# Performance work log

Measured on AMD Instinct MI355X. Metric: run time of the kernel, lower is better.

## Reference

```python
import jax, jax.numpy as jnp
import numpy as np

N = 30000      # nodes
E = 480000     # edges
H = 128        # hidden_nf
NQ = 7         # qubits
D = 2 ** NQ    # 128, quantum state dim == embedding_size
NL = 2         # block n_layers (QGCL layers)
QL = 2         # quantum circuit layers inside each QGCL
NORM = 100.0   # normalization_factor ('sum' aggregation)
NORM_CONST = 1.0


def _cnot_perm_indices(n):
    # Composed permutation for CNOT(0,1)...CNOT(n-2,n-1), CNOT(n-1,0).
    # PennyLane convention: wire 0 is the most significant bit.
    idx = np.arange(2 ** n)
    pairs = [(i, i + 1) for i in range(n - 1)] + [(n - 1, 0)]
    g = None
    for c, t in pairs:
        cb = (idx >> (n - 1 - c)) & 1
        f = idx ^ (cb << (n - 1 - t))  # flip target bit if control set (involution)
        g = f if g is None else g[f]
    return g

_CNOT_G = jnp.asarray(_cnot_perm_indices(NQ))


def _quantum_states(q_in, coeffs, A_re, A_im):
    """Vectorized VQC over all nodes. q_in [N,D] real -> [N,D] complex state."""
    norm = jnp.sqrt(jnp.sum(q_in ** 2, axis=1, keepdims=True) + 1e-12)
    s = (q_in / norm).astype(jnp.complex64)  # normalized initial state per node
    I = jnp.eye(D, dtype=jnp.complex64)
    for j in range(QL):
        # Cayley transform -> unitary
        A = (A_re[j] + 1j * A_im[j]).astype(jnp.complex64)
        A = A + A.conj().T
        q = (A - 1j * I) @ jnp.linalg.inv(A + 1j * I)
        # single-qubit layer: RY(b) @ RX(a) on every qubit -> kron power
        a, b = coeffs[j, 0].astype(jnp.complex64), coeffs[j, 1].astype(jnp.complex64)
        ca, sa = jnp.cos(a / 2), jnp.sin(a / 2)
        cb, sb = jnp.cos(b / 2), jnp.sin(b / 2)
        RX = jnp.stack([jnp.stack([ca, -1j * sa]), jnp.stack([-1j * sa, ca])])
        RY = jnp.stack([jnp.stack([cb, -sb]), jnp.stack([sb, cb])])
        G = RY @ RX
        Gk = G
        for _ in range(NQ - 1):
            Gk = jnp.kron(Gk, G)
        s = s @ q.T            # QubitUnitary
        s = s @ Gk.T           # RX/RY on all qubits
        s = s[:, _CNOT_G]      # CNOT ring (pure permutation)
    return s


def setup_inputs() -> dict:
    key = jax.random.key(0)
    ks = jax.random.split(key, 20)
    return {
        "h": jax.random.normal(ks[0], (N, H), jnp.float32),
        "x": jax.random.normal(ks[1], (N, 3), jnp.float32),
        "edge_index": jax.random.randint(ks[2], (2, E), 0, N, jnp.int32),
        "edge_attr": jax.random.normal(ks[3], (E, 1), jnp.float32),
        "e_w1": jax.random.normal(ks[4], (NL, 2 * H + 2, H), jnp.float32) * 0.05,
        "e_b1": jnp.zeros((NL, H), jnp.float32),
        "e_w2": jax.random.normal(ks[5], (NL, H, H), jnp.float32) * 0.05,
        "e_b2": jnp.zeros((NL, H), jnp.float32),
        "enc_w": jax.random.normal(ks[6], (NL, 2 * H, D), jnp.float32) * 0.05,
        "enc_b": jnp.zeros((NL, D), jnp.float32),
        "coeffs": jax.random.normal(ks[7], (NL, QL, 2), jnp.float32) * 0.1,
        "A_re": jax.random.normal(ks[8], (NL, QL, D, D), jnp.float32) * 0.01,
        "A_im": jax.random.normal(ks[9], (NL, QL, D, D), jnp.float32) * 0.01,
        "dec_w": jax.random.normal(ks[10], (NL, D, H), jnp.float32) * 0.05,
        "dec_b": jnp.zeros((NL, H), jnp.float32),
        "c_w1": jax.random.normal(ks[11], (2 * H + 2, H), jnp.float32) * 0.05,
        "c_b1": jnp.zeros((H,), jnp.float32),
        "c_w2": jax.random.normal(ks[12], (H, H), jnp.float32) * 0.05,
        "c_b2": jnp.zeros((H,), jnp.float32),
        "c_w3": jax.random.normal(ks[13], (H, 1), jnp.float32) * 0.001,  # xavier gain=0.001
    }


def reference(h, x, edge_index, edge_attr, e_w1, e_b1, e_w2, e_b2, enc_w, enc_b,
              coeffs, A_re, A_im, dec_w, dec_b, c_w1, c_b1, c_w2, c_b2, c_w3):
    row, col = edge_index[0], edge_index[1]
    # coord2diff
    diff = x[row] - x[col]
    radial = jnp.sum(diff ** 2, axis=1, keepdims=True)     # [E,1] (used as 'distances')
    coord_diff = diff / (jnp.sqrt(radial + 1e-8) + NORM_CONST)
    eattr = jnp.concatenate([radial, edge_attr], axis=1)   # [E,2]

    for l in range(NL):  # QGCL layers
        m = jnp.concatenate([h[row], h[col], eattr], axis=1)       # [E, 2H+2]
        m = jax.nn.silu(m @ e_w1[l] + e_b1[l])
        m = jax.nn.silu(m @ e_w2[l] + e_b2[l])                     # edge messages mij
        agg = jax.ops.segment_sum(m, row, num_segments=N) / NORM   # scatter-add
        q_in = jnp.concatenate([h, agg], axis=1) @ enc_w[l] + enc_b[l]
        # quantum part is detached in the original (torch .detach + re-tensor)
        qs = jax.lax.stop_gradient(
            _quantum_states(q_in, coeffs[l], A_re[l], A_im[l]))
        h = h + qs.real.astype(h.dtype) @ dec_w[l] + dec_b[l]

    # EquivariantUpdate (tanh=False)
    t = jnp.concatenate([h[row], h[col], eattr], axis=1)
    t = jax.nn.silu(t @ c_w1 + c_b1)
    t = jax.nn.silu(t @ c_w2 + c_b2)
    t = t @ c_w3                                                   # [E,1]
    trans = coord_diff * t
    x = x + jax.ops.segment_sum(trans, row, num_segments=N) / NORM
    return h, x
```

## Files before the change

### kernel.cpp

```cpp
#include <hip/hip_runtime.h>
#include <math.h>

#define N_NODES 30000
#define N_EDGES 480000
#define HDIM 128
#define EPB 64
#define NAS 264
#define MS 136
#define M2S 132

typedef __attribute__((ext_vector_type(8))) short short8b;
typedef __attribute__((ext_vector_type(4))) float f32x4;

__device__ __forceinline__ float silu_f(float v) {
  return v / (1.0f + __expf(-v));
}

__device__ __forceinline__ unsigned short f2bf(float f) {
  unsigned int u = __float_as_uint(f);
  unsigned int r = u + 0x7fffu + ((u >> 16) & 1u);
  return (unsigned short)(r >> 16);
}

__device__ __forceinline__ unsigned int cvt_pk_bf16(float lo, float hi) {
  unsigned int r;
  asm("v_cvt_pk_bf16_f32 %0, %1, %2" : "=v"(r) : "v"(lo), "v"(hi));
  return r;
}

__global__ void init_out_bf_kernel(const float* __restrict__ h,
                                   const float* __restrict__ x,
                                   const int* __restrict__ ei,
                                   float* __restrict__ out,
                                   ushort* __restrict__ hbf,
                                   int* __restrict__ cursor) {
  int idx = blockIdx.x * 256 + threadIdx.x;
  float4 v = ((const float4*)h)[idx];
  ((float4*)out)[idx] = v;
  ushort4 o;
  o.x = f2bf(v.x); o.y = f2bf(v.y); o.z = f2bf(v.z); o.w = f2bf(v.w);
  ((ushort4*)hbf)[idx] = o;
  if (idx < N_NODES * 3 / 4) {
    ((float4*)(out + N_NODES * HDIM))[idx] = ((const float4*)x)[idx];
  }
  if (idx < N_EDGES) atomicAdd(&cursor[ei[idx]], 1);
}

__global__ __launch_bounds__(1024) void scan_kernel(int* __restrict__ cursor,
                                                    int* __restrict__ cstart) {
  __shared__ int sums[1024];
  const int tid = threadIdx.x;
  const int base = tid * 30;
  int local[30];
  int s = 0;
#pragma unroll
  for (int j = 0; j < 30; ++j) {
    int idx = base + j;
    int d = (idx < N_NODES) ? cursor[idx] : 0;
    local[j] = s;
    s += d;
  }
  sums[tid] = s;
  __syncthreads();
  for (int off = 1; off < 1024; off <<= 1) {
    int add = (tid >= off) ? sums[tid - off] : 0;
    __syncthreads();
    sums[tid] += add;
    __syncthreads();
  }
  int excl = (tid == 0) ? 0 : sums[tid - 1];
#pragma unroll
  for (int j = 0; j < 30; ++j) {
    int idx = base + j;
    if (idx < N_NODES) {
      int v = excl + local[j];
      cursor[idx] = v;
      cstart[idx] = v;
    }
  }
}

__global__ void prep_kernel(
    const int* __restrict__ ei, int* __restrict__ cursor, int* __restrict__ elist,
    const float* __restrict__ e_w1, const float* __restrict__ e_w2,
    const float* __restrict__ enc_w, const float* __restrict__ c_w1,
    const float* __restrict__ c_w2,
    ushort* __restrict__ w1cs, ushort* __restrict__ w2cs,
    ushort* __restrict__ enccs, ushort* __restrict__ cw1cs,
    ushort* __restrict__ cw2cs,
    const float* __restrict__ A_re, const float* __restrict__ A_im,
    float2* __restrict__ X,
    const float* __restrict__ coeffs, float2* __restrict__ gkm) {
  const int b = blockIdx.x, tid = threadIdx.x;
  if (b < 1875) {
    int e = b * 256 + tid;
    int r = ei[e];
    int pos = atomicAdd(&cursor[r], 1);
    elist[pos] = e;
  } else if (b < 2755) {
    int idx = (b - 1875) * 256 + tid;
    int ci = idx >> 12, rem = idx & 4095, kk = rem & 31;
    const float* W; ushort* dst; int Kreal, ktl;
    if (ci < 18) {
      int l = ci / 9; ktl = ci - l * 9;
      W = e_w1 + (size_t)l * 258 * HDIM; dst = w1cs + (size_t)l * 9 * 4096;
      Kreal = 258;
    } else if (ci < 26) {
      int c2 = ci - 18; int l = c2 >> 2; ktl = c2 & 3;
      W = e_w2 + (size_t)l * HDIM * HDIM; dst = w2cs + (size_t)l * 4 * 4096;
      Kreal = 128;
    } else if (ci < 42) {
      int c2 = ci - 26; int l = c2 >> 3; ktl = c2 & 7;
      W = enc_w + (size_t)l * 256 * HDIM; dst = enccs + (size_t)l * 8 * 4096;
      Kreal = 256;
    } else if (ci < 51) {
      ktl = ci - 42; W = c_w1; dst = cw1cs; Kreal = 258;
    } else {
      ktl = ci - 51; W = c_w2; dst = cw2cs; Kreal = 128;
    }
    int n = rem >> 5;
    int k = ktl * 32 + kk;
    float v = (k < Kreal) ? W[(size_t)k * HDIM + n] : 0.0f;
    dst[ktl * 4096 + rem] = f2bf(v);
  } else if (b < 3011) {
    int bb = b - 2755;
    int lj = bb >> 6;
    int idx = (bb & 63) * 256 + tid;
    int r = idx >> 7, c = idx & 127;
    const float* are = A_re + (size_t)lj * 16384;
    const float* aim = A_im + (size_t)lj * 16384;
    float re = are[r * 128 + c] + are[c * 128 + r];
    float im = aim[r * 128 + c] - aim[c * 128 + r];
    if (r == c) im -= 1.0f;
    X[(size_t)lj * 16384 + idx] = make_float2(re, im);
  } else {
    int bb = b - 3011;
    int lj = bb >> 6;
    float a = coeffs[lj * 2 + 0], bcf = coeffs[lj * 2 + 1];
    float ca = cosf(0.5f * a), sa = sinf(0.5f * a);
    float cb = cosf(0.5f * bcf), sb = sinf(0.5f * bcf);
    float2 G[2][2];
    G[0][0] = make_float2(cb * ca, sb * sa);
    G[0][1] = make_float2(-sb * ca, -cb * sa);
    G[1][0] = make_float2(sb * ca, -cb * sa);
    G[1][1] = make_float2(cb * ca, -sb * sa);
    int idx = (bb & 63) * 256 + tid;
    int r = idx >> 7, c = idx & 127;
    float2 acc = make_float2(1.f, 0.f);
#pragma unroll
    for (int bit = 6; bit >= 0; --bit) {
      float2 g = G[(r >> bit) & 1][(c >> bit) & 1];
      acc = make_float2(acc.x * g.x - acc.y * g.y, acc.x * g.y + acc.y * g.x);
    }
    gkm[(size_t)lj * 16384 + idx] = acc;
  }
}

__global__ void ns_bx_kernel(const float* __restrict__ Are,
                             const float* __restrict__ Aim,
                             const float2* __restrict__ X,
                             float2* __restrict__ T) {
  int lj = blockIdx.y;
  int idx = blockIdx.x * 256 + threadIdx.x;
  int r = idx >> 7, c = idx & 127;
  const float* are = Are + (size_t)lj * 16384;
  const float* aim = Aim + (size_t)lj * 16384;
  const float2* x = X + (size_t)lj * 16384;
  float2 acc = make_float2(0.f, 0.f);
  for (int k = 0; k < 128; ++k) {
    float re = are[r * 128 + k] + are[k * 128 + r];
    float im = aim[r * 128 + k] - aim[k * 128 + r];
    if (k == r) im += 1.0f;
    float2 b = x[k * 128 + c];
    acc.x += re * b.x - im * b.y;
    acc.y += re * b.y + im * b.x;
  }
  T[(size_t)lj * 16384 + idx] = acc;
}

__global__ void ns_upd_kernel(const float2* __restrict__ X,
                              const float2* __restrict__ T,
                              float2* __restrict__ Xn) {
  int lj = blockIdx.y;
  int idx = blockIdx.x * 256 + threadIdx.x;
  int r = idx >> 7, c = idx & 127;
  const float2* x = X + (size_t)lj * 16384;
  const float2* t = T + (size_t)lj * 16384;
  float2 acc = make_float2(0.f, 0.f);
  for (int k = 0; k < 128; ++k) {
    float2 a = x[r * 128 + k];
    float2 b = t[k * 128 + c];
    acc.x += a.x * b.x - a.y * b.y;
    acc.y += a.x * b.y + a.y * b.x;
  }
  float2 xc = x[r * 128 + c];
  Xn[(size_t)lj * 16384 + idx] = make_float2(2.f * xc.x - acc.x, 2.f * xc.y - acc.y);
}

__global__ void qmat_kernel(const float* __restrict__ Are,
                            const float* __restrict__ Aim,
                            const float2* __restrict__ binvg,
                            float2* __restrict__ qm) {
  int lj = blockIdx.y;
  int idx = blockIdx.x * 256 + threadIdx.x;
  int r = idx >> 7, c = idx & 127;
  const float* are = Are + (size_t)lj * 16384;
  const float* aim = Aim + (size_t)lj * 16384;
// ... 20 lines not shown
  {
    int v = c;
    const int cs[7] = {6, 5, 4, 3, 2, 1, 0};
    const int ts[7] = {0, 6, 5, 4, 3, 2, 1};
#pragma unroll
    for (int p = 0; p < 7; ++p) {
      int cb = (v >> (6 - cs[p])) & 1;
      v = v ^ (cb << (6 - ts[p]));
    }
    gc = v;
  }
  const float2* q = qm + (size_t)lj * 16384;
  const float2* gk = gkm + (size_t)lj * 16384;
  float2 acc = make_float2(0.f, 0.f);
  for (int k = 0; k < 128; ++k) {
    float2 qa = q[k * 128 + i];
    float2 gb = gk[gc * 128 + k];
    acc.x += qa.x * gb.x - qa.y * gb.y;
    acc.y += qa.x * gb.y + qa.y * gb.x;
  }
  njm[(size_t)lj * 16384 + idx] = acc;
}

__global__ void compose_kernel(const float2* __restrict__ njm,
                               float2* __restrict__ um) {
  int l = blockIdx.y;
  int idx = blockIdx.x * 256 + threadIdx.x;
  int i = idx >> 7, c = idx & 127;
  const float2* n0 = njm + (size_t)(l * 2 + 0) * 16384;
  const float2* n1 = njm + (size_t)(l * 2 + 1) * 16384;
  float2 acc = make_float2(0.f, 0.f);
  for (int k = 0; k < 128; ++k) {
    float2 a = n0[i * 128 + k];
    float2 b = n1[k * 128 + c];
    acc.x += a.x * b.x - a.y * b.y;
    acc.y += a.x * b.y + a.y * b.x;
  }
  um[(size_t)l * 16384 + idx] = acc;
}

__global__ void wqd_kernel(const float2* __restrict__ um,
                           const float* __restrict__ decw,
                           ushort* __restrict__ wqdcs) {
  int l = blockIdx.y;
  int idx = blockIdx.x * 256 + threadIdx.x;
  int i = idx >> 7, c = idx & 127;
  const float2* u = um + (size_t)l * 16384;
  const float* dw = decw + (size_t)l * 16384;
  float acc = 0.f;
  for (int k = 0; k < 128; ++k) acc += u[i * 128 + k].x * dw[k * 128 + c];
  wqdcs[(size_t)l * 4 * 4096 + (i >> 5) * 4096 + c * 32 + (i & 31)] = f2bf(acc);
}

__global__ __launch_bounds__(256, 1) void pgemm_kernel(
    const ushort* __restrict__ hbf, const ushort* __restrict__ wcs,
    const float* __restrict__ b1, ushort* __restrict__ P) {
  __shared__ ushort Ht[EPB * MS];
  const int tid = threadIdx.x;
  const int n0 = blockIdx.x * EPB;
  const int lane = tid & 63, wave = tid >> 6;
  const int lrow = lane & 15, lq = lane >> 4;

  {
    const int e = tid >> 2, jj = tid & 3;
    int node = n0 + e;
    if (node >= N_NODES) node = N_NODES - 1;
    const uint4* src = (const uint4*)(hbf + (size_t)node * HDIM + jj * 32);
    uint4* dst = (uint4*)(Ht + e * MS + jj * 32);
    dst[0] = src[0]; dst[1] = src[1]; dst[2] = src[2]; dst[3] = src[3];
  }
  short8b wf[4][4];
  const int cs = (wave >> 1) * 4;
  const int nb = (wave & 1) * 64;
#pragma unroll
  for (int kt = 0; kt < 4; ++kt)
#pragma unroll
    for (int nt = 0; nt < 4; ++nt)
      wf[kt][nt] = *(const short8b*)(wcs + (cs + kt) * 4096 + (nb + nt * 16 + lrow) * 32 + lq * 8);
  __syncthreads();

  f32x4 acc[4][4];
#pragma unroll
  for (int mt = 0; mt < 4; ++mt)
#pragma unroll
    for (int nt = 0; nt < 4; ++nt) acc[mt][nt] = (f32x4){0.f, 0.f, 0.f, 0.f};
#pragma unroll
  for (int kt = 0; kt < 4; ++kt) {
    short8b af[4];
#pragma unroll
    for (int mt = 0; mt < 4; ++mt)
      af[mt] = *(const short8b*)(Ht + (mt * 16 + lrow) * MS + kt * 32 + lq * 8);
#pragma unroll
    for (int mt = 0; mt < 4; ++mt)
#pragma unroll
      for (int nt = 0; nt < 4; ++nt)
        acc[mt][nt] = __builtin_amdgcn_mfma_f32_16x16x32_bf16(af[mt], wf[kt][nt], acc[mt][nt], 0, 0, 0);
  }
  const int cbase = wave * 64;
#pragma unroll
  for (int nt = 0; nt < 4; ++nt) {
    const int ccol = cbase + nt * 16 + lrow;
    const float bb = (ccol < 128) ? b1[ccol] : 0.f;
#pragma unroll
    for (int mt = 0; mt < 4; ++mt)
#pragma unroll
      for (int r = 0; r < 4; ++r) {
        const int node = n0 + mt * 16 + lq * 4 + r;
        if (node < N_NODES) P[(size_t)node * 256 + ccol] = f2bf(acc[mt][nt][r] + bb);
      }
  }
}

__global__ __launch_bounds__(256, 4) void edge_mfma_kernel(
    const ushort* __restrict__ P, const int* __restrict__ ei,
    const float* __restrict__ x, const float* __restrict__ ea,
    const int* __restrict__ elist, const int* __restrict__ cstart,
    const float* __restrict__ wm,
    const ushort* __restrict__ w2cs, const float* __restrict__ b2,
    float* __restrict__ agg, float* __restrict__ headp) {
  __shared__ float m2s[EPB * M2S];
  __shared__ int rows[EPB];
  ushort* m1 = (ushort*)m2s;

  const int tid = threadIdx.x;
  const int lane = tid & 63, wave = tid >> 6;
  const int lrow = lane & 15, lq = lane >> 4;
  const int wbase = wave * 32;
  const int woff0 = (wbase + lrow) * 32 + lq * 8;
  const int woff1 = (wbase + 16 + lrow) * 32 + lq * 8;
  const float b2v[2] = {b2[wbase + lrow], b2[wbase + 16 + lrow]};

  const int i0 = blockIdx.x * EPB;
  {
    const int e = tid >> 2, j = tid & 3;
    const int edge = elist[i0 + e];
    const int r = ei[edge], c = ei[N_EDGES + edge];
    if (j == 0) rows[e] = r;
    const uint4* pr = (const uint4*)(P + (size_t)r * 256 + j * 32);
    const uint4* pc = (const uint4*)(P + (size_t)c * 256 + 128 + j * 32);
    uint4 PR[4] = {pr[0], pr[1], pr[2], pr[3]};
    uint4 PC[4] = {pc[0], pc[1], pc[2], pc[3]};
    float dx = x[r * 3 + 0] - x[c * 3 + 0];
    float dy = x[r * 3 + 1] - x[c * 3 + 1];
    float dz = x[r * 3 + 2] - x[c * 3 + 2];
    float radial = dx * dx + dy * dy + dz * dz;
    float eav = ea[edge];
#pragma unroll
    for (int q = 0; q < 4; ++q) {
      const int kb = j * 32 + q * 8;
      const uint ua[4] = {PR[q].x, PR[q].y, PR[q].z, PR[q].w};
      const uint ub[4] = {PC[q].x, PC[q].y, PC[q].z, PC[q].w};
      uint ow[4];
#pragma unroll
      for (int w = 0; w < 4; ++w) {
        const int k = kb + w * 2;
        float v0 = __uint_as_float(ua[w] << 16) + __uint_as_float(ub[w] << 16)
                 + radial * wm[k] + eav * wm[128 + k];
        float v1 = __uint_as_float(ua[w] & 0xffff0000u) + __uint_as_float(ub[w] & 0xffff0000u)
                 + radial * wm[k + 1] + eav * wm[129 + k];
        ow[w] = cvt_pk_bf16(silu_f(v0), silu_f(v1));
      }
      uint4 o; o.x = ow[0]; o.y = ow[1]; o.z = ow[2]; o.w = ow[3];
      *(uint4*)(m1 + e * MS + kb) = o;
    }
  }
  __syncthreads();

  f32x4 acc2[4][2];
#pragma unroll
  for (int mt = 0; mt < 4; ++mt)
#pragma unroll
    for (int nt = 0; nt < 2; ++nt) acc2[mt][nt] = (f32x4){0.f, 0.f, 0.f, 0.f};
  {
    short8b wcur0 = *(const short8b*)(w2cs + woff0);
    short8b wcur1 = *(const short8b*)(w2cs + woff1);
#pragma unroll
    for (int kt = 0; kt < 4; ++kt) {
      short8b wn0, wn1;
      if (kt < 3) {
        wn0 = *(const short8b*)(w2cs + (kt + 1) * 4096 + woff0);
        wn1 = *(const short8b*)(w2cs + (kt + 1) * 4096 + woff1);
      }
      short8b af[4];
#pragma unroll
      for (int mt = 0; mt < 4; ++mt)
        af[mt] = *(const short8b*)(m1 + (mt * 16 + lrow) * MS + kt * 32 + lq * 8);
#pragma unroll
      for (int mt = 0; mt < 4; ++mt) {
        acc2[mt][0] = __builtin_amdgcn_mfma_f32_16x16x32_bf16(af[mt], wcur0, acc2[mt][0], 0, 0, 0);
        acc2[mt][1] = __builtin_amdgcn_mfma_f32_16x16x32_bf16(af[mt], wcur1, acc2[mt][1], 0, 0, 0);
      }
      if (kt < 3) { wcur0 = wn0; wcur1 = wn1; }
    }
  }
  __syncthreads();
#pragma unroll
  for (int mt = 0; mt < 4; ++mt)
#pragma unroll
    for (int nt = 0; nt < 2; ++nt)
#pragma unroll
      for (int r = 0; r < 4; ++r)
        m2s[(mt * 16 + lq * 4 + r) * M2S + wbase + nt * 16 + lrow] =
            silu_f(acc2[mt][nt][r] + b2v[nt]);
  __syncthreads();

  const int e2 = tid & 63, cg = tid >> 6, cb = cg * 32;
  if (((e2 & 1) == 0) && (rows[e2 + 1] == rows[e2])) {
    float* d = m2s + e2 * M2S + cb;
    const float* s = m2s + (e2 + 1) * M2S + cb;
#pragma unroll
    for (int q = 0; q < 8; ++q)
      *(f32x4*)(d + q * 4) = *(const f32x4*)(d + q * 4) + *(const f32x4*)(s + q * 4);
  }
  __syncthreads();
  if (((e2 & 3) == 0) && (rows[e2 + 2] == rows[e2])) {
    float* d = m2s + e2 * M2S + cb;
    const float* s = m2s + (e2 + 2) * M2S + cb;
#pragma unroll
    for (int q = 0; q < 8; ++q)
      *(f32x4*)(d + q * 4) = *(const f32x4*)(d + q * 4) + *(const f32x4*)(s + q * 4);
  }
  __syncthreads();
  const int r_e = rows[e2];
  const bool leader = (e2 == 0) || (rows[e2 - 1] != r_e);
  if (leader) {
    f32x4 sum[8];
#pragma unroll
    for (int q = 0; q < 8; ++q) sum[q] = *(const f32x4*)(m2s + e2 * M2S + cb + q * 4);
    int f = e2 + ((e2 & 1) ? 1 : ((e2 & 2) ? 2 : 4));
    while (f < EPB && rows[f] == r_e) {
#pragma unroll
      for (int q = 0; q < 8; ++q) sum[q] += *(const f32x4*)(m2s + f * M2S + cb + q * 4);
      f += (f & 1) ? 1 : ((f & 2) ? 2 : 4);
    }
    float* dst = (e2 == 0 && cstart[r_e] < i0)
                     ? headp + (size_t)blockIdx.x * HDIM + cb
                     : agg + (size_t)r_e * HDIM + cb;
#pragma unroll
    for (int q = 0; q < 8; ++q) *(f32x4*)(dst + q * 4) = sum[q];
  }
}

__global__ __launch_bounds__(256, 2) void node_mfma_kernel(
    float* __restrict__ out_h, const float* __restrict__ agg,
    const int* __restrict__ cstart, const int* __restrict__ cend,
    const float* __restrict__ headp,
    const ushort* __restrict__ enccs, const float* __restrict__ encb,
    const ushort* __restrict__ wqdcs, const float* __restrict__ decb,
    ushort* __restrict__ hbf) {
  __shared__ ushort A[EPB * NAS];
  __shared__ ushort m1[EPB * MS];
  __shared__ float nbuf[4 * EPB];
  const int tid = threadIdx.x;
  const int n0 = blockIdx.x * EPB;

  const int lane = tid & 63, wave = tid >> 6;
  const int lrow = lane & 15, lq = lane >> 4;
  const int wbase = wave * 32;

  short8b wef[8][2], wqf[4][2];
#pragma unroll
  for (int kt = 0; kt < 8; ++kt)
#pragma unroll
    for (int nt = 0; nt < 2; ++nt)
      wef[kt][nt] = *(const short8b*)(enccs + kt * 4096 + (wbase + nt * 16 + lrow) * 32 + lq * 8);
#pragma unroll
  for (int kt = 0; kt < 4; ++kt)
#pragma unroll
    for (int nt = 0; nt < 2; ++nt)
      wqf[kt][nt] = *(const short8b*)(wqdcs + kt * 4096 + (wbase + nt * 16 + lrow) * 32 + lq * 8);
  const float ebv[2] = {encb[wbase + lrow], encb[wbase + 16 + lrow]};
  const float dbv[2] = {decb[wbase + lrow], decb[wbase + 16 + lrow]};

  {
    const int e = tid >> 2, j = tid & 3;
    int node = n0 + e;
    if (node >= N_NODES) node = N_NODES - 1;
    if (j < 2) {
      const float4* s4 = (const float4*)(out_h + (size_t)node * HDIM + j * 64);
      ushort* dst = A + e * NAS + j * 64;
#pragma unroll
      for (int i = 0; i < 16; ++i) {
        float4 v = s4[i];
        ushort4 o;
        o.x = f2bf(v.x); o.y = f2bf(v.y); o.z = f2bf(v.z); o.w = f2bf(v.w);
        ((ushort4*)dst)[i] = o;
      }
    } else {
      const int s = cstart[node], en = cend[node];
      const bool hasAgg = en > s;
      const float4* a4 = (const float4*)(agg + (size_t)node * HDIM + (j - 2) * 64);
      const int bb0 = (s >> 6) + 1;
      const int bb1 = hasAgg ? ((en - 1) >> 6) : 0;
      ushort* dst = A + e * NAS + 128 + (j - 2) * 64;
#pragma unroll
      for (int i = 0; i < 16; ++i) {
        float4 v = hasAgg ? a4[i] : make_float4(0.f, 0.f, 0.f, 0.f);
        for (int bb = bb0; bb <= bb1; ++bb) {
          float4 hv = *(const float4*)(headp + (size_t)bb * HDIM + (j - 2) * 64 + i * 4);
          v.x += hv.x; v.y += hv.y; v.z += hv.z; v.w += hv.w;
        }
        ushort4 o;
// ... 23 lines not shown
        acc[mt][nt] = __builtin_amdgcn_mfma_f32_16x16x32_bf16(af[mt], wef[kt][nt], acc[mt][nt], 0, 0, 0);
  }
#pragma unroll
  for (int mt = 0; mt < 4; ++mt) {
    float ssp[4] = {0.f, 0.f, 0.f, 0.f};
#pragma unroll
    for (int nt = 0; nt < 2; ++nt)
#pragma unroll
      for (int r = 0; r < 4; ++r) {
        acc[mt][nt][r] += ebv[nt];
        ssp[r] += acc[mt][nt][r] * acc[mt][nt][r];
      }
#pragma unroll
    for (int m = 1; m < 16; m <<= 1)
#pragma unroll
      for (int r = 0; r < 4; ++r) ssp[r] += __shfl_xor(ssp[r], m, 64);
    if (lrow == 0) {
#pragma unroll
      for (int r = 0; r < 4; ++r)
        nbuf[wave * EPB + mt * 16 + lq * 4 + r] = ssp[r];
    }
  }
  __syncthreads();
#pragma unroll
  for (int mt = 0; mt < 4; ++mt)
#pragma unroll
    for (int r = 0; r < 4; ++r) {
      const int row = mt * 16 + lq * 4 + r;
      float sum = nbuf[row] + nbuf[EPB + row] + nbuf[2 * EPB + row] + nbuf[3 * EPB + row];
      float inv = 1.0f / sqrtf(sum + 1e-12f);
#pragma unroll
      for (int nt = 0; nt < 2; ++nt)
        m1[row * MS + wbase + nt * 16 + lrow] = f2bf(acc[mt][nt][r] * inv);
    }
  __syncthreads();

  f32x4 acc2[4][2];
#pragma unroll
  for (int mt = 0; mt < 4; ++mt)
#pragma unroll
    for (int nt = 0; nt < 2; ++nt) acc2[mt][nt] = (f32x4){0.f, 0.f, 0.f, 0.f};
#pragma unroll
  for (int kt = 0; kt < 4; ++kt) {
    short8b af[4];
#pragma unroll
    for (int mt = 0; mt < 4; ++mt)
      af[mt] = *(const short8b*)(m1 + (mt * 16 + lrow) * MS + kt * 32 + lq * 8);
#pragma unroll
    for (int mt = 0; mt < 4; ++mt)
#pragma unroll
      for (int nt = 0; nt < 2; ++nt)
        acc2[mt][nt] = __builtin_amdgcn_mfma_f32_16x16x32_bf16(af[mt], wqf[kt][nt], acc2[mt][nt], 0, 0, 0);
  }
#pragma unroll
  for (int mt = 0; mt < 4; ++mt)
#pragma unroll
    for (int nt = 0; nt < 2; ++nt) {
      const int n = wbase + nt * 16 + lrow;
#pragma unroll
      for (int r = 0; r < 4; ++r) {
        const int node = n0 + mt * 16 + lq * 4 + r;
        if (node < N_NODES) {
          size_t off = (size_t)node * HDIM + n;
          float hn = out_h[off] + acc2[mt][nt][r] + dbv[nt];
          out_h[off] = hn;
          hbf[off] = f2bf(hn);
        }
      }
    }
}

__global__ __launch_bounds__(256, 4) void coord_mfma_kernel(
    const ushort* __restrict__ P, const int* __restrict__ ei,
    const float* __restrict__ x, const float* __restrict__ ea,
    const int* __restrict__ elist,
    const float* __restrict__ wm,
    const ushort* __restrict__ w2cs, const float* __restrict__ b2,
    const float* __restrict__ w3, float* __restrict__ xout) {
  __shared__ ushort m1[EPB * MS];
  __shared__ int rows[EPB];
  __shared__ float pbuf[4 * EPB];
  __shared__ float tv[EPB];
  __shared__ float dxs[EPB], dys[EPB], dzs[EPB], ses[EPB];

  const int tid = threadIdx.x;
  const int lane = tid & 63, wave = tid >> 6;
  const int lrow = lane & 15, lq = lane >> 4;
  const int wbase = wave * 32;
  const int woff0 = (wbase + lrow) * 32 + lq * 8;
  const int woff1 = (wbase + 16 + lrow) * 32 + lq * 8;

  const float b2v[2] = {b2[wbase + lrow], b2[wbase + 16 + lrow]};
  const float w3v[2] = {w3[wbase + lrow], w3[wbase + 16 + lrow]};

  const int i0 = blockIdx.x * EPB;
  {
    const int e = tid >> 2, j = tid & 3;
    const int edge = elist[i0 + e];
    const int r = ei[edge], c = ei[N_EDGES + edge];
    if (j == 0) rows[e] = r;
    const uint4* pr = (const uint4*)(P + (size_t)r * 256 + j * 32);
    const uint4* pc = (const uint4*)(P + (size_t)c * 256 + 128 + j * 32);
    uint4 PR[4] = {pr[0], pr[1], pr[2], pr[3]};
    uint4 PC[4] = {pc[0], pc[1], pc[2], pc[3]};
    float dx = x[r * 3 + 0] - x[c * 3 + 0];
    float dy = x[r * 3 + 1] - x[c * 3 + 1];
    float dz = x[r * 3 + 2] - x[c * 3 + 2];
    float radial = dx * dx + dy * dy + dz * dz;
    float eav = ea[edge];
    if (j == 3) {
      dxs[e] = dx; dys[e] = dy; dzs[e] = dz;
      ses[e] = 1.0f / (sqrtf(radial + 1e-8f) + 1.0f);
    }
#pragma unroll
    for (int q = 0; q < 4; ++q) {
      const int kb = j * 32 + q * 8;
      const uint ua[4] = {PR[q].x, PR[q].y, PR[q].z, PR[q].w};
      const uint ub[4] = {PC[q].x, PC[q].y, PC[q].z, PC[q].w};
      uint ow[4];
#pragma unroll
      for (int w = 0; w < 4; ++w) {
        const int k = kb + w * 2;
        float v0 = __uint_as_float(ua[w] << 16) + __uint_as_float(ub[w] << 16)
                 + radial * wm[k] + eav * wm[128 + k];
        float v1 = __uint_as_float(ua[w] & 0xffff0000u) + __uint_as_float(ub[w] & 0xffff0000u)
                 + radial * wm[k + 1] + eav * wm[129 + k];
        ow[w] = cvt_pk_bf16(silu_f(v0), silu_f(v1));
      }
      uint4 o; o.x = ow[0]; o.y = ow[1]; o.z = ow[2]; o.w = ow[3];
      *(uint4*)(m1 + e * MS + kb) = o;
    }
  }
  __syncthreads();

  f32x4 acc2[4][2];
#pragma unroll
  for (int mt = 0; mt < 4; ++mt)
#pragma unroll
    for (int nt = 0; nt < 2; ++nt) acc2[mt][nt] = (f32x4){0.f, 0.f, 0.f, 0.f};
  {
    short8b wcur0 = *(const short8b*)(w2cs + woff0);
    short8b wcur1 = *(const short8b*)(w2cs + woff1);
#pragma unroll
    for (int kt = 0; kt < 4; ++kt) {
      short8b wn0, wn1;
      if (kt < 3) {
        wn0 = *(const short8b*)(w2cs + (kt + 1) * 4096 + woff0);
        wn1 = *(const short8b*)(w2cs + (kt + 1) * 4096 + woff1);
      }
      short8b af[4];
#pragma unroll
      for (int mt = 0; mt < 4; ++mt)
        af[mt] = *(const short8b*)(m1 + (mt * 16 + lrow) * MS + kt * 32 + lq * 8);
#pragma unroll
      for (int mt = 0; mt < 4; ++mt) {
        acc2[mt][0] = __builtin_amdgcn_mfma_f32_16x16x32_bf16(af[mt], wcur0, acc2[mt][0], 0, 0, 0);
        acc2[mt][1] = __builtin_amdgcn_mfma_f32_16x16x32_bf16(af[mt], wcur1, acc2[mt][1], 0, 0, 0);
      }
      if (kt < 3) { wcur0 = wn0; wcur1 = wn1; }
    }
  }
#pragma unroll
  for (int mt = 0; mt < 4; ++mt) {
// ... 15 lines not shown
  }
  __syncthreads();
  if (tid < EPB) {
    tv[tid] = (pbuf[tid] + pbuf[EPB + tid] + pbuf[2 * EPB + tid] + pbuf[3 * EPB + tid])
              * 0.01f * ses[tid];
  }
  __syncthreads();
  if (tid < EPB) {
    const int e = tid;
    const int r_e = rows[e];
    const bool leader = (e == 0) || (rows[e - 1] != r_e);
    if (leader) {
      float sx = 0.f, sy = 0.f, sz = 0.f;
      int f = e;
      do {
        float t = tv[f];
        sx += dxs[f] * t; sy += dys[f] * t; sz += dzs[f] * t;
        ++f;
      } while (f < EPB && rows[f] == r_e);
      atomicAdd(&xout[r_e * 3 + 0], sx);
      atomicAdd(&xout[r_e * 3 + 1], sy);
      atomicAdd(&xout[r_e * 3 + 2], sz);
    }
  }
}

extern "C" void kernel_launch(void* const* d_in, const int* in_sizes, int n_in,
                              void* d_out, int out_size, void* d_ws, size_t ws_size,
                              hipStream_t stream) {
  const float* h     = (const float*)d_in[0];
  const float* x     = (const float*)d_in[1];
  const int*   ei    = (const int*)d_in[2];
  const float* ea    = (const float*)d_in[3];
  const float* e_w1  = (const float*)d_in[4];
  const float* e_b1  = (const float*)d_in[5];
  const float* e_w2  = (const float*)d_in[6];
  const float* e_b2  = (const float*)d_in[7];
  const float* enc_w = (const float*)d_in[8];
  const float* enc_b = (const float*)d_in[9];
  const float* coeffs= (const float*)d_in[10];
  const float* A_re  = (const float*)d_in[11];
  const float* A_im  = (const float*)d_in[12];
  const float* dec_w = (const float*)d_in[13];
  const float* dec_b = (const float*)d_in[14];
  const float* c_w1  = (const float*)d_in[15];
  const float* c_b1  = (const float*)d_in[16];
  const float* c_w2  = (const float*)d_in[17];
  const float* c_b2  = (const float*)d_in[18];
  const float* c_w3  = (const float*)d_in[19];

  float* out = (float*)d_out;
  float* ws  = (float*)d_ws;

  float*  agg    = ws;
  float2* xa     = (float2*)(ws + 3840000);
  float2* xb     = (float2*)(ws + 3971072);
  float2* xt     = (float2*)(ws + 4102144);
  float2* qm     = (float2*)(ws + 4233216);
  float2* gkm    = (float2*)(ws + 4364288);
  float2* njm    = (float2*)(ws + 4495360);
  float2* um     = (float2*)(ws + 4626432);
  int*    cursor = (int*)(ws + 4724864);
  int*    cstart = (int*)(ws + 4754864);
  int*    elist  = (int*)(ws + 4784864);
  float*  headp  = ws + 5264864;
  ushort* hbf    = (ushort*)(ws + 6224864);
  ushort* w1cs   = (ushort*)(ws + 8144864);
  ushort* w2cs   = (ushort*)(ws + 8181728);
  ushort* cw1cs  = (ushort*)(ws + 8198112);
  ushort* cw2cs  = (ushort*)(ws + 8216544);
  ushort* enccs  = (ushort*)(ws + 8224736);
  ushort* wqdcs  = (ushort*)(ws + 8257504);
  ushort* Pbuf   = (ushort*)(ws + 8273888);

  hipMemsetAsync(cursor, 0, N_NODES * sizeof(int), stream);
  init_out_bf_kernel<<<3750, 256, 0, stream>>>(h, x, ei, out, hbf, cursor);
  scan_kernel<<<1, 1024, 0, stream>>>(cursor, cstart);

  prep_kernel<<<3267, 256, 0, stream>>>(ei, cursor, elist,
                                        e_w1, e_w2, enc_w, c_w1, c_w2,
                                        w1cs, w2cs, enccs, cw1cs, cw2cs,
                                        A_re, A_im, xa, coeffs, gkm);

  float2* cur = xa;
  float2* nxt = xb;
  for (int it = 0; it < 2; ++it) {
    ns_bx_kernel<<<dim3(64, 4), 256, 0, stream>>>(A_re, A_im, cur, xt);
    ns_upd_kernel<<<dim3(64, 4), 256, 0, stream>>>(cur, xt, nxt);
    float2* tmp = cur; cur = nxt; nxt = tmp;
  }
  qmat_kernel<<<dim3(64, 4), 256, 0, stream>>>(A_re, A_im, cur, qm);
  nj_kernel<<<dim3(64, 4), 256, 0, stream>>>(qm, gkm, njm);
  compose_kernel<<<dim3(64, 2), 256, 0, stream>>>(njm, um);
  wqd_kernel<<<dim3(64, 2), 256, 0, stream>>>(um, dec_w, wqdcs);

  const int NB = (N_NODES + EPB - 1) / EPB;

  for (int l = 0; l < 2; ++l) {
    pgemm_kernel<<<NB, 256, 0, stream>>>(hbf, w1cs + (size_t)l * 9 * 4096,
                                         e_b1 + l * HDIM, Pbuf);
    edge_mfma_kernel<<<N_EDGES / EPB, 256, 0, stream>>>(
        Pbuf, ei, x, ea, elist, cstart,
        e_w1 + (size_t)l * 258 * HDIM + 256 * HDIM,
        w2cs + (size_t)l * 4 * 4096, e_b2 + l * HDIM, agg, headp);
    node_mfma_kernel<<<NB, 256, 0, stream>>>(
        out, agg, cstart, cursor, headp,
        enccs + (size_t)l * 8 * 4096, enc_b + l * HDIM,
        wqdcs + (size_t)l * 4 * 4096, dec_b + l * HDIM, hbf);
  }

  pgemm_kernel<<<NB, 256, 0, stream>>>(hbf, cw1cs, c_b1, Pbuf);
  coord_mfma_kernel<<<N_EDGES / EPB, 256, 0, stream>>>(
      Pbuf, ei, x, ea, elist, c_w1 + 256 * HDIM, cw2cs, c_b2, c_w3,
      out + (size_t)N_NODES * HDIM);
}
```

Measured before the change: 697.7 us.

## Fuse node projections into prep/node kernels, pack edge data, MFMA segment reduce

Removes the standalone pgemm kernel. The first projection now runs as extra blocks in prep_kernel, and the later ones run at the tail of node_mfma_kernel, which writes the next P buffer directly. Edge sorting now stores packed row/col indices and precomputed radial/edge_attr pairs in sorted order, so the edge kernels skip the indirection and the x gathers. The edge kernel's shared-memory tree reduction by row is replaced with a bf16 one-hot segment-sum matrix multiply on MFMA. The messages are now summed in bf16 rather than fp32 before aggregation, which adds some precision loss.

```diff
diff --git a/kernel.cpp b/kernel.cpp
--- a/kernel.cpp
+++ b/kernel.cpp
@@ -7,7 +7,7 @@
 #define EPB 64
 #define NAS 264
 #define MS 136
-#define M2S 132
+#define M2TS 72
 
 typedef __attribute__((ext_vector_type(8))) short short8b;
 typedef __attribute__((ext_vector_type(4))) float f32x4;
@@ -32,14 +32,9 @@
                                    const float* __restrict__ x,
                                    const int* __restrict__ ei,
                                    float* __restrict__ out,
-                                   ushort* __restrict__ hbf,
                                    int* __restrict__ cursor) {
   int idx = blockIdx.x * 256 + threadIdx.x;
-  float4 v = ((const float4*)h)[idx];
-  ((float4*)out)[idx] = v;
-  ushort4 o;
-  o.x = f2bf(v.x); o.y = f2bf(v.y); o.z = f2bf(v.z); o.w = f2bf(v.w);
-  ((ushort4*)hbf)[idx] = o;
+  ((float4*)out)[idx] = ((const float4*)h)[idx];
   if (idx < N_NODES * 3 / 4) {
     ((float4*)(out + N_NODES * HDIM))[idx] = ((const float4*)x)[idx];
   }
@@ -81,7 +76,9 @@
 }
 
 __global__ void prep_kernel(
-    const int* __restrict__ ei, int* __restrict__ cursor, int* __restrict__ elist,
+    const int* __restrict__ ei, int* __restrict__ cursor,
+    unsigned int* __restrict__ rcp, float2* __restrict__ era,
+    const float* __restrict__ x, const float* __restrict__ ea,
     const float* __restrict__ e_w1, const float* __restrict__ e_w2,
     const float* __restrict__ enc_w, const float* __restrict__ c_w1,
     const float* __restrict__ c_w2,
@@ -90,13 +87,21 @@
     ushort* __restrict__ cw2cs,
     const float* __restrict__ A_re, const float* __restrict__ A_im,
     float2* __restrict__ X,
-    const float* __restrict__ coeffs, float2* __restrict__ gkm) {
+    const float* __restrict__ coeffs, float2* __restrict__ gkm,
+    const float* __restrict__ outh, const float* __restrict__ b1l0,
+    ushort* __restrict__ P) {
+  __shared__ ushort Ht[EPB * MS];
   const int b = blockIdx.x, tid = threadIdx.x;
   if (b < 1875) {
     int e = b * 256 + tid;
     int r = ei[e];
+    int c = ei[N_EDGES + e];
     int pos = atomicAdd(&cursor[r], 1);
-    elist[pos] = e;
+    rcp[pos] = (unsigned int)r | ((unsigned int)c << 16);
+    float dx = x[r * 3 + 0] - x[c * 3 + 0];
+    float dy = x[r * 3 + 1] - x[c * 3 + 1];
+    float dz = x[r * 3 + 2] - x[c * 3 + 2];
+    era[pos] = make_float2(dx * dx + dy * dy + dz * dz, ea[e]);
   } else if (b < 2755) {
     int idx = (b - 1875) * 256 + tid;
     int ci = idx >> 12, rem = idx & 4095, kk = rem & 31;
@@ -133,7 +138,7 @@
     float im = aim[r * 128 + c] - aim[c * 128 + r];
     if (r == c) im -= 1.0f;
     X[(size_t)lj * 16384 + idx] = make_float2(re, im);
-  } else {
+  } else if (b < 3267) {
     int bb = b - 3011;
     int lj = bb >> 6;
     float a = coeffs[lj * 2 + 0], bcf = coeffs[lj * 2 + 1];
@@ -153,6 +158,64 @@
       acc = make_float2(acc.x * g.x - acc.y * g.y, acc.x * g.y + acc.y * g.x);
     }
     gkm[(size_t)lj * 16384 + idx] = acc;
+  } else {
+    const int n0 = (b - 3267) * EPB;
+    const int lane = tid & 63, wave = tid >> 6;
+    const int lrow = lane & 15, lq = lane >> 4;
+    {
+      const int e = tid >> 2, jj = tid & 3;
+      int node = n0 + e;
+      if (node >= N_NODES) node = N_NODES - 1;
+      const float4* s4 = (const float4*)(outh + (size_t)node * HDIM + jj * 32);
+      ushort* dst = Ht + e * MS + jj * 32;
+#pragma unroll
+      for (int i = 0; i < 8; ++i) {
+        float4 v = s4[i];
+        ushort4 o;
+        o.x = f2bf(v.x); o.y = f2bf(v.y); o.z = f2bf(v.z); o.w = f2bf(v.w);
+        ((ushort4*)dst)[i] = o;
+      }
+    }
+    short8b wf[4][4];
+    const int cs = (wave >> 1) * 4;
+    const int nb = (wave & 1) * 64;
+#pragma unroll
+    for (int kt = 0; kt < 4; ++kt)
+#pragma unroll
+      for (int nt = 0; nt < 4; ++nt)
+        wf[kt][nt] = *(const short8b*)(w1cs + (cs + kt) * 4096 + (nb + nt * 16 + lrow) * 32 + lq * 8);
+    __syncthreads();
+
+    f32x4 acc[4][4];
+#pragma unroll
+    for (int mt = 0; mt < 4; ++mt)
+#pragma unroll
+      for (int nt = 0; nt < 4; ++nt) acc[mt][nt] = (f32x4){0.f, 0.f, 0.f, 0.f};
+#pragma unroll
+    for (int kt = 0; kt < 4; ++kt) {
+      short8b af[4];
+#pragma unroll
+      for (int mt = 0; mt < 4; ++mt)
+        af[mt] = *(const short8b*)(Ht + (mt * 16 + lrow) * MS + kt * 32 + lq * 8);
+#pragma unroll
+      for (int mt = 0; mt < 4; ++mt)
+#pragma unroll
+        for (int nt = 0; nt < 4; ++nt)
+          acc[mt][nt] = __builtin_amdgcn_mfma_f32_16x16x32_bf16(af[mt], wf[kt][nt], acc[mt][nt], 0, 0, 0);
+    }
+    const int cbase = wave * 64;
+#pragma unroll
+    for (int nt = 0; nt < 4; ++nt) {
+      const int ccol = cbase + nt * 16 + lrow;
+      const float bb2 = (ccol < 128) ? b1l0[ccol] : 0.f;
+#pragma unroll
+      for (int mt = 0; mt < 4; ++mt)
+#pragma unroll
+        for (int r = 0; r < 4; ++r) {
+          const int node = n0 + mt * 16 + lq * 4 + r;
+          if (node < N_NODES) P[(size_t)node * 256 + ccol] = f2bf(acc[mt][nt][r] + bb2);
+        }
+    }
   }
 }
 
@@ -279,75 +342,19 @@
   wqdcs[(size_t)l * 4 * 4096 + (i >> 5) * 4096 + c * 32 + (i & 31)] = f2bf(acc);
 }
 
-__global__ __launch_bounds__(256, 1) void pgemm_kernel(
-    const ushort* __restrict__ hbf, const ushort* __restrict__ wcs,
-    const float* __restrict__ b1, ushort* __restrict__ P) {
-  __shared__ ushort Ht[EPB * MS];
-  const int tid = threadIdx.x;
-  const int n0 = blockIdx.x * EPB;
-  const int lane = tid & 63, wave = tid >> 6;
-  const int lrow = lane & 15, lq = lane >> 4;
-
-  {
-    const int e = tid >> 2, jj = tid & 3;
-    int node = n0 + e;
-    if (node >= N_NODES) node = N_NODES - 1;
-    const uint4* src = (const uint4*)(hbf + (size_t)node * HDIM + jj * 32);
-    uint4* dst = (uint4*)(Ht + e * MS + jj * 32);
-    dst[0] = src[0]; dst[1] = src[1]; dst[2] = src[2]; dst[3] = src[3];
-  }
-  short8b wf[4][4];
-  const int cs = (wave >> 1) * 4;
-  const int nb = (wave & 1) * 64;
-#pragma unroll
-  for (int kt = 0; kt < 4; ++kt)
-#pragma unroll
-    for (int nt = 0; nt < 4; ++nt)
-      wf[kt][nt] = *(const short8b*)(wcs + (cs + kt) * 4096 + (nb + nt * 16 + lrow) * 32 + lq * 8);
-  __syncthreads();
-
-  f32x4 acc[4][4];
-#pragma unroll
-  for (int mt = 0; mt < 4; ++mt)
-#pragma unroll
-    for (int nt = 0; nt < 4; ++nt) acc[mt][nt] = (f32x4){0.f, 0.f, 0.f, 0.f};
-#pragma unroll
-  for (int kt = 0; kt < 4; ++kt) {
-    short8b af[4];
-#pragma unroll
-    for (int mt = 0; mt < 4; ++mt)
-      af[mt] = *(const short8b*)(Ht + (mt * 16 + lrow) * MS + kt * 32 + lq * 8);
-#pragma unroll
-    for (int mt = 0; mt < 4; ++mt)
-#pragma unroll
-      for (int nt = 0; nt < 4; ++nt)
-        acc[mt][nt] = __builtin_amdgcn_mfma_f32_16x16x32_bf16(af[mt], wf[kt][nt], acc[mt][nt], 0, 0, 0);
-  }
-  const int cbase = wave * 64;
-#pragma unroll
-  for (int nt = 0; nt < 4; ++nt) {
-    const int ccol = cbase + nt * 16 + lrow;
-    const float bb = (ccol < 128) ? b1[ccol] : 0.f;
-#pragma unroll
-    for (int mt = 0; mt < 4; ++mt)
-#pragma unroll
-      for (int r = 0; r < 4; ++r) {
-        const int node = n0 + mt * 16 + lq * 4 + r;
-        if (node < N_NODES) P[(size_t)node * 256 + ccol] = f2bf(acc[mt][nt][r] + bb);
-      }
-  }
-}
-
 __global__ __launch_bounds__(256, 4) void edge_mfma_kernel(
-    const ushort* __restrict__ P, const int* __restrict__ ei,
-    const float* __restrict__ x, const float* __restrict__ ea,
-    const int* __restrict__ elist, const int* __restrict__ cstart,
+    const ushort* __restrict__ P, const unsigned int* __restrict__ rcp,
+    const float2* __restrict__ era, const int* __restrict__ cstart,
     const float* __restrict__ wm,
     const ushort* __restrict__ w2cs, const float* __restrict__ b2,
     float* __restrict__ agg, float* __restrict__ headp) {
-  __shared__ float m2s[EPB * M2S];
+  __shared__ ushort buf[128 * M2TS];
   __shared__ int rows[EPB];
-  ushort* m1 = (ushort*)m2s;
+  __shared__ __align__(16) ushort segv[EPB];
+  __shared__ int segnode[EPB];
+  __shared__ int scont, snseg;
+  ushort* m1 = buf;
+  ushort* m2t = buf;
 
   const int tid = threadIdx.x;
   const int lane = tid & 63, wave = tid >> 6;
@@ -360,18 +367,15 @@
   const int i0 = blockIdx.x * EPB;
   {
     const int e = tid >> 2, j = tid & 3;
-    const int edge = elist[i0 + e];
-    const int r = ei[edge], c = ei[N_EDGES + edge];
+    const unsigned int rcv = rcp[i0 + e];
+    const int r = (int)(rcv & 0xFFFFu), c = (int)(rcv >> 16);
     if (j == 0) rows[e] = r;
+    const float2 re2 = era[i0 + e];
+    const float radial = re2.x, eav = re2.y;
     const uint4* pr = (const uint4*)(P + (size_t)r * 256 + j * 32);
     const uint4* pc = (const uint4*)(P + (size_t)c * 256 + 128 + j * 32);
     uint4 PR[4] = {pr[0], pr[1], pr[2], pr[3]};
     uint4 PC[4] = {pc[0], pc[1], pc[2], pc[3]};
-    float dx = x[r * 3 + 0] - x[c * 3 + 0];
-    float dy = x[r * 3 + 1] - x[c * 3 + 1];
-    float dz = x[r * 3 + 2] - x[c * 3 + 2];
-    float radial = dx * dx + dy * dy + dz * dz;
-    float eav = ea[edge];
 #pragma unroll
     for (int q = 0; q < 4; ++q) {
       const int kb = j * 32 + q * 8;
@@ -421,50 +425,86 @@
     }
   }
   __syncthreads();
+
 #pragma unroll
   for (int mt = 0; mt < 4; ++mt)
 #pragma unroll
-    for (int nt = 0; nt < 2; ++nt)
-#pragma unroll
-      for (int r = 0; r < 4; ++r)
-        m2s[(mt * 16 + lq * 4 + r) * M2S + wbase + nt * 16 + lrow] =
-            silu_f(acc2[mt][nt][r] + b2v[nt]);
-  __syncthreads();
-
-  const int e2 = tid & 63, cg = tid >> 6, cb = cg * 32;
-  if (((e2 & 1) == 0) && (rows[e2 + 1] == rows[e2])) {
-    float* d = m2s + e2 * M2S + cb;
-    const float* s = m2s + (e2 + 1) * M2S + cb;
-#pragma unroll
-    for (int q = 0; q < 8; ++q)
-      *(f32x4*)(d + q * 4) = *(const f32x4*)(d + q * 4) + *(const f32x4*)(s + q * 4);
-  }
-  __syncthreads();
-  if (((e2 & 3) == 0) && (rows[e2 + 2] == rows[e2])) {
-    float* d = m2s + e2 * M2S + cb;
-    const float* s = m2s + (e2 + 2) * M2S + cb;
-#pragma unroll
-    for (int q = 0; q < 8; ++q)
-      *(f32x4*)(d + q * 4) = *(const f32x4*)(d + q * 4) + *(const f32x4*)(s + q * 4);
-  }
-  __syncthreads();
-  const int r_e = rows[e2];
-  const bool leader = (e2 == 0) || (rows[e2 - 1] != r_e);
-  if (leader) {
-    f32x4 sum[8];
-#pragma unroll
-    for (int q = 0; q < 8; ++q) sum[q] = *(const f32x4*)(m2s + e2 * M2S + cb + q * 4);
-    int f = e2 + ((e2 & 1) ? 1 : ((e2 & 2) ? 2 : 4));
-    while (f < EPB && rows[f] == r_e) {
-#pragma unroll
-      for (int q = 0; q < 8; ++q) sum[q] += *(const f32x4*)(m2s + f * M2S + cb + q * 4);
-      f += (f & 1) ? 1 : ((f & 2) ? 2 : 4);
-    }
-    float* dst = (e2 == 0 && cstart[r_e] < i0)
-                     ? headp + (size_t)blockIdx.x * HDIM + cb
-                     : agg + (size_t)r_e * HDIM + cb;
-#pragma unroll
-    for (int q = 0; q < 8; ++q) *(f32x4*)(dst + q * 4) = sum[q];
+    for (int nt = 0; nt < 2; ++nt) {
+      const int col = wbase + nt * 16 + lrow;
+#pragma unroll
+      for (int r = 0; r < 4; ++r) {
+        const int e = mt * 16 + lq * 4 + r;
+        m2t[col * M2TS + e] = f2bf(silu_f(acc2[mt][nt][r] + b2v[nt]));
+      }
+    }
+  if (wave == 0) {
+    const int e = lane;
+    const int re_ = rows[e];
+    const bool leader = (e == 0) || (rows[e - 1] != re_);
+    const unsigned long long mask = __ballot(leader);
+    const int seg = (int)__popcll(mask & ((1ull << e) - 1ull));
+    segv[e] = (ushort)seg;
+    if (leader) segnode[seg] = re_;
+    if (e == 0) {
+      snseg = (int)__popcll(mask);
+      scont = (cstart[re_] < i0) ? 1 : 0;
+    }
+  }
+  __syncthreads();
+
+  const int nseg = snseg, cont = scont;
+  const int ntmax = (nseg + 15) >> 4;
+  const short8b sv0 = *(const short8b*)(segv + lq * 8);
+  const short8b sv1 = *(const short8b*)(segv + 32 + lq * 8);
+  const int mtb = wave * 32;
+  short8b afr[2][2];
+#pragma unroll
+  for (int mt = 0; mt < 2; ++mt) {
+    const ushort* rp = m2t + (mtb + mt * 16 + lrow) * M2TS + lq * 8;
+    afr[mt][0] = *(const short8b*)(rp);
+    afr[mt][1] = *(const short8b*)(rp + 32);
+  }
+  f32x4 racc[2][4];
+#pragma unroll
+  for (int mt = 0; mt < 2; ++mt)
+#pragma unroll
+    for (int nt = 0; nt < 4; ++nt) racc[mt][nt] = (f32x4){0.f, 0.f, 0.f, 0.f};
+#pragma unroll
+  for (int nt = 0; nt < 4; ++nt) {
+    if (nt >= ntmax) continue;
+    const int tgt = nt * 16 + lrow;
+    uint p0[4], p1[4];
+#pragma unroll
+    for (int w = 0; w < 4; ++w) {
+      p0[w] = (((int)(ushort)sv0[2 * w] == tgt) ? 0x3F80u : 0u)
+            | (((int)(ushort)sv0[2 * w + 1] == tgt) ? 0x3F800000u : 0u);
+      p1[w] = (((int)(ushort)sv1[2 * w] == tgt) ? 0x3F80u : 0u)
+            | (((int)(ushort)sv1[2 * w + 1] == tgt) ? 0x3F800000u : 0u);
+    }
+    uint4 u0 = make_uint4(p0[0], p0[1], p0[2], p0[3]);
+    uint4 u1 = make_uint4(p1[0], p1[1], p1[2], p1[3]);
+    const short8b bf0 = *(const short8b*)&u0;
+    const short8b bf1 = *(const short8b*)&u1;
+#pragma unroll
+    for (int mt = 0; mt < 2; ++mt) {
+      racc[mt][nt] = __builtin_amdgcn_mfma_f32_16x16x32_bf16(afr[mt][0], bf0, racc[mt][nt], 0, 0, 0);
+      racc[mt][nt] = __builtin_amdgcn_mfma_f32_16x16x32_bf16(afr[mt][1], bf1, racc[mt][nt], 0, 0, 0);
+    }
+  }
+#pragma unroll
+  for (int nt = 0; nt < 4; ++nt) {
+    if (nt >= ntmax) continue;
+    const int seg = nt * 16 + lrow;
+    if (seg < nseg) {
+      const int node = segnode[seg];
+      float* dst = (seg == 0 && cont) ? (headp + (size_t)blockIdx.x * HDIM)
+                                      : (agg + (size_t)node * HDIM);
+#pragma unroll
+      for (int mt = 0; mt < 2; ++mt)
+#pragma unroll
+        for (int r = 0; r < 4; ++r)
+          dst[mtb + mt * 16 + lq * 4 + r] = racc[mt][nt][r];
+    }
   }
 }
 
@@ -474,7 +514,8 @@
     const float* __restrict__ headp,
     const ushort* __restrict__ enccs, const float* __restrict__ encb,
     const ushort* __restrict__ wqdcs, const float* __restrict__ decb,
-    ushort* __restrict__ hbf) {
+    const ushort* __restrict__ w1n, const float* __restrict__ b1n,
+    ushort* __restrict__ Pout) {
   __shared__ ushort A[EPB * NAS];
   __shared__ ushort m1[EPB * MS];
   __shared__ float nbuf[4 * EPB];
@@ -604,6 +645,8 @@
       for (int nt = 0; nt < 2; ++nt)
         acc2[mt][nt] = __builtin_amdgcn_mfma_f32_16x16x32_bf16(af[mt], wqf[kt][nt], acc2[mt][nt], 0, 0, 0);
   }
+  __syncthreads();
+
 #pragma unroll
   for (int mt = 0; mt < 4; ++mt)
 #pragma unroll
@@ -612,20 +655,60 @@
 #pragma unroll
       for (int r = 0; r < 4; ++r) {
         const int node = n0 + mt * 16 + lq * 4 + r;
+        float hn = 0.f;
         if (node < N_NODES) {
           size_t off = (size_t)node * HDIM + n;
-          float hn = out_h[off] + acc2[mt][nt][r] + dbv[nt];
+          hn = out_h[off] + acc2[mt][nt][r] + dbv[nt];
           out_h[off] = hn;
-          hbf[off] = f2bf(hn);
         }
-      }
-    }
+        m1[(mt * 16 + lq * 4 + r) * MS + n] = f2bf(hn);
+      }
+    }
+  __syncthreads();
+
+  short8b wfp[4][4];
+  const int csn = (wave >> 1) * 4;
+  const int nbw = (wave & 1) * 64;
+#pragma unroll
+  for (int kt = 0; kt < 4; ++kt)
+#pragma unroll
+    for (int nt = 0; nt < 4; ++nt)
+      wfp[kt][nt] = *(const short8b*)(w1n + (csn + kt) * 4096 + (nbw + nt * 16 + lrow) * 32 + lq * 8);
+  f32x4 pacc[4][4];
+#pragma unroll
+  for (int mt = 0; mt < 4; ++mt)
+#pragma unroll
+    for (int nt = 0; nt < 4; ++nt) pacc[mt][nt] = (f32x4){0.f, 0.f, 0.f, 0.f};
+#pragma unroll
+  for (int kt = 0; kt < 4; ++kt) {
+    short8b af[4];
+#pragma unroll
+    for (int mt = 0; mt < 4; ++mt)
+      af[mt] = *(const short8b*)(m1 + (mt * 16 + lrow) * MS + kt * 32 + lq * 8);
+#pragma unroll
+    for (int mt = 0; mt < 4; ++mt)
+#pragma unroll
+      for (int nt = 0; nt < 4; ++nt)
+        pacc[mt][nt] = __builtin_amdgcn_mfma_f32_16x16x32_bf16(af[mt], wfp[kt][nt], pacc[mt][nt], 0, 0, 0);
+  }
+  const int cbase = wave * 64;
+#pragma unroll
+  for (int nt = 0; nt < 4; ++nt) {
+    const int ccol = cbase + nt * 16 + lrow;
+    const float bb2 = (ccol < 128) ? b1n[ccol] : 0.f;
+#pragma unroll
+    for (int mt = 0; mt < 4; ++mt)
+#pragma unroll
+      for (int r = 0; r < 4; ++r) {
+        const int node = n0 + mt * 16 + lq * 4 + r;
+        if (node < N_NODES) Pout[(size_t)node * 256 + ccol] = f2bf(pacc[mt][nt][r] + bb2);
+      }
+  }
 }
 
 __global__ __launch_bounds__(256, 4) void coord_mfma_kernel(
-    const ushort* __restrict__ P, const int* __restrict__ ei,
-    const float* __restrict__ x, const float* __restrict__ ea,
-    const int* __restrict__ elist,
+    const ushort* __restrict__ P, const unsigned int* __restrict__ rcp,
+    const float2* __restrict__ era, const float* __restrict__ x,
     const float* __restrict__ wm,
     const ushort* __restrict__ w2cs, const float* __restrict__ b2,
     const float* __restrict__ w3, float* __restrict__ xout) {
@@ -648,19 +731,19 @@
   const int i0 = blockIdx.x * EPB;
   {
     const int e = tid >> 2, j = tid & 3;
-    const int edge = elist[i0 + e];
-    const int r = ei[edge], c = ei[N_EDGES + edge];
+    const unsigned int rcv = rcp[i0 + e];
+    const int r = (int)(rcv & 0xFFFFu), c = (int)(rcv >> 16);
     if (j == 0) rows[e] = r;
+    const float2 re2 = era[i0 + e];
+    const float radial = re2.x, eav = re2.y;
     const uint4* pr = (const uint4*)(P + (size_t)r * 256 + j * 32);
     const uint4* pc = (const uint4*)(P + (size_t)c * 256 + 128 + j * 32);
     uint4 PR[4] = {pr[0], pr[1], pr[2], pr[3]};
     uint4 PC[4] = {pc[0], pc[1], pc[2], pc[3]};
-    float dx = x[r * 3 + 0] - x[c * 3 + 0];
-    float dy = x[r * 3 + 1] - x[c * 3 + 1];
-    float dz = x[r * 3 + 2] - x[c * 3 + 2];
-    float radial = dx * dx + dy * dy + dz * dz;
-    float eav = ea[edge];
     if (j == 3) {
+      float dx = x[r * 3 + 0] - x[c * 3 + 0];
+      float dy = x[r * 3 + 1] - x[c * 3 + 1];
+      float dz = x[r * 3 + 2] - x[c * 3 + 2];
       dxs[e] = dx; dys[e] = dy; dzs[e] = dz;
       ses[e] = 1.0f / (sqrtf(radial + 1e-8f) + 1.0f);
     }
@@ -782,35 +865,36 @@
   float* out = (float*)d_out;
   float* ws  = (float*)d_ws;
 
-  float*  agg    = ws;
-  float2* xa     = (float2*)(ws + 3840000);
-  float2* xb     = (float2*)(ws + 3971072);
-  float2* xt     = (float2*)(ws + 4102144);
-  float2* qm     = (float2*)(ws + 4233216);
-  float2* gkm    = (float2*)(ws + 4364288);
-  float2* njm    = (float2*)(ws + 4495360);
-  float2* um     = (float2*)(ws + 4626432);
-  int*    cursor = (int*)(ws + 4724864);
-  int*    cstart = (int*)(ws + 4754864);
-  int*    elist  = (int*)(ws + 4784864);
-  float*  headp  = ws + 5264864;
-  ushort* hbf    = (ushort*)(ws + 6224864);
-  ushort* w1cs   = (ushort*)(ws + 8144864);
-  ushort* w2cs   = (ushort*)(ws + 8181728);
-  ushort* cw1cs  = (ushort*)(ws + 8198112);
-  ushort* cw2cs  = (ushort*)(ws + 8216544);
-  ushort* enccs  = (ushort*)(ws + 8224736);
-  ushort* wqdcs  = (ushort*)(ws + 8257504);
-  ushort* Pbuf   = (ushort*)(ws + 8273888);
+  float*        agg    = ws;
+  float2*       xa     = (float2*)(ws + 3840000);
+  float2*       xb     = (float2*)(ws + 3971072);
+  float2*       xt     = (float2*)(ws + 4102144);
+  float2*       qm     = (float2*)(ws + 4233216);
+  float2*       gkm    = (float2*)(ws + 4364288);
+  float2*       njm    = (float2*)(ws + 4495360);
+  float2*       um     = (float2*)(ws + 4626432);
+  int*          cursor = (int*)(ws + 4724864);
+  int*          cstart = (int*)(ws + 4754864);
+  unsigned int* rcp    = (unsigned int*)(ws + 4784864);
+  float2*       era    = (float2*)(ws + 5264864);
+  float*        headp  = ws + 6224864;
+  ushort*       w1cs   = (ushort*)(ws + 7184864);
+  ushort*       w2cs   = (ushort*)(ws + 7221728);
+  ushort*       cw1cs  = (ushort*)(ws + 7238112);
+  ushort*       cw2cs  = (ushort*)(ws + 7256544);
+  ushort*       enccs  = (ushort*)(ws + 7264736);
+  ushort*       wqdcs  = (ushort*)(ws + 7297504);
+  ushort*       Pbuf   = (ushort*)(ws + 7313888);
 
   hipMemsetAsync(cursor, 0, N_NODES * sizeof(int), stream);
-  init_out_bf_kernel<<<3750, 256, 0, stream>>>(h, x, ei, out, hbf, cursor);
+  init_out_bf_kernel<<<3750, 256, 0, stream>>>(h, x, ei, out, cursor);
   scan_kernel<<<1, 1024, 0, stream>>>(cursor, cstart);
 
-  prep_kernel<<<3267, 256, 0, stream>>>(ei, cursor, elist,
+  prep_kernel<<<3736, 256, 0, stream>>>(ei, cursor, rcp, era, x, ea,
                                         e_w1, e_w2, enc_w, c_w1, c_w2,
                                         w1cs, w2cs, enccs, cw1cs, cw2cs,
-                                        A_re, A_im, xa, coeffs, gkm);
+                                        A_re, A_im, xa, coeffs, gkm,
+                                        out, e_b1, Pbuf);
 
   float2* cur = xa;
   float2* nxt = xb;
@@ -827,20 +911,20 @@
   const int NB = (N_NODES + EPB - 1) / EPB;
 
   for (int l = 0; l < 2; ++l) {
-    pgemm_kernel<<<NB, 256, 0, stream>>>(hbf, w1cs + (size_t)l * 9 * 4096,
-                                         e_b1 + l * HDIM, Pbuf);
     edge_mfma_kernel<<<N_EDGES / EPB, 256, 0, stream>>>(
-        Pbuf, ei, x, ea, elist, cstart,
+        Pbuf, rcp, era, cstart,
         e_w1 + (size_t)l * 258 * HDIM + 256 * HDIM,
         w2cs + (size_t)l * 4 * 4096, e_b2 + l * HDIM, agg, headp);
     node_mfma_kernel<<<NB, 256, 0, stream>>>(
         out, agg, cstart, cursor, headp,
         enccs + (size_t)l * 8 * 4096, enc_b + l * HDIM,
-        wqdcs + (size_t)l * 4 * 4096, dec_b + l * HDIM, hbf);
-  }
-
-  pgemm_kernel<<<NB, 256, 0, stream>>>(hbf, cw1cs, c_b1, Pbuf);
+        wqdcs + (size_t)l * 4 * 4096, dec_b + l * HDIM,
+        (l == 0) ? (w1cs + (size_t)9 * 4096) : cw1cs,
+        (l == 0) ? (e_b1 + HDIM) : c_b1,
+        Pbuf);
+  }
+
   coord_mfma_kernel<<<N_EDGES / EPB, 256, 0, stream>>>(
-      Pbuf, ei, x, ea, elist, c_w1 + 256 * HDIM, cw2cs, c_b2, c_w3,
+      Pbuf, rcp, era, x, c_w1 + 256 * HDIM, cw2cs, c_b2, c_w3,
       out + (size_t)N_NODES * HDIM);
 }
```

New measurement: 672.9 us. -3.6%, faster.
